# Kernel optimization log

Hardware: AMD Instinct MI355X
Metric: run time of the kernel (lower is better)

The kernel has to match this reference:

```python
import jax, jax.numpy as jnp
import numpy as np


def setup_inputs() -> dict:
    key = jax.random.key(0)
    x = jax.random.uniform(key, (16, 3, 224, 224), dtype=jnp.float32)
    return {"x": x, "timesteps": 32, "burst_length": 3, "interburst_interval": 5}


def reference(x, timesteps, burst_length, interburst_interval):
    period = burst_length + interburst_interval  # 8
    max_bursts = timesteps // period             # 4
    x_norm = jnp.clip(x, 0.0, 1.0)
    # floor(x * max_bursts) == torch .long() cast for non-negative values
    n_bursts = jnp.floor(x_norm * max_bursts)    # [B, *input_shape], float

    t = jnp.arange(timesteps)                    # [T]
    burst_idx = (t // period).astype(x.dtype)    # which burst each timestep belongs to
    within_burst = (t % period) < burst_length   # [T] bool

    # reshape time axis to broadcast at position 1: [1, T, 1, ..., 1]
    tshape = (1, timesteps) + (1,) * (x.ndim - 1)
    burst_idx = burst_idx.reshape(tshape)
    within_burst = within_burst.reshape(tshape)

    nb = jnp.expand_dims(n_bursts, 1)            # [B, 1, *input_shape]
    spikes = (within_burst & (burst_idx < nb)).astype(jnp.float32)
    return spikes  # [B, T, *input_shape]
```

## Files before the change

kernel.cpp:

```cpp
#include <hip/hip_runtime.h>


__global__ __launch_bounds__(256) void burst_coding_kernel(
    const float* __restrict__ x, float* __restrict__ out,
    const int* __restrict__ p_bl, const int* __restrict__ p_ibi,
    int T, int S4)
{
    const int bl     = *p_bl;
    const int period = bl + *p_ibi;
    const int maxb   = T / period;

    const int bt   = blockIdx.y;
    const int t    = bt % T;
    const int b    = bt / T;
    const int tm   = t % period;
    const int bidx = t / period;

    const int s4 = blockIdx.x * blockDim.x + threadIdx.x;
    if (s4 >= S4) return;

    float4* op = reinterpret_cast<float4*>(out) + (long)bt * S4 + s4;

    if (tm >= bl || bidx >= maxb) {
        *op = make_float4(0.f, 0.f, 0.f, 0.f);
        return;
    }

    const float mbf  = (float)maxb;
    const float bthr = (float)(bidx + 1);
    const float4 xv  = reinterpret_cast<const float4*>(x)[(long)b * S4 + s4];

    float4 v;
    v.x = (fminf(fmaxf(xv.x, 0.f), 1.f) * mbf >= bthr) ? 1.f : 0.f;
    v.y = (fminf(fmaxf(xv.y, 0.f), 1.f) * mbf >= bthr) ? 1.f : 0.f;
    v.z = (fminf(fmaxf(xv.z, 0.f), 1.f) * mbf >= bthr) ? 1.f : 0.f;
    v.w = (fminf(fmaxf(xv.w, 0.f), 1.f) * mbf >= bthr) ? 1.f : 0.f;
    *op = v;
}

extern "C" void kernel_launch(void* const* d_in, const int* in_sizes, int n_in,
                              void* d_out, int out_size, void* d_ws, size_t ws_size,
                              hipStream_t stream) {
    const float* x   = (const float*)d_in[0];
    const int* p_bl  = (const int*)d_in[2];
    const int* p_ibi = (const int*)d_in[3];
    float* out = (float*)d_out;

    const long N  = (long)in_sizes[0];
    const int  T  = (int)((long)out_size / N);
    const int  S  = 3 * 224 * 224;
    const int  S4 = S / 4;
    const int  B  = (int)(N / S);

    const int threads = 256;
    dim3 grid((S4 + threads - 1) / threads,
              (unsigned)(B * T));

    burst_coding_kernel<<<grid, dim3(threads), 0, stream>>>(
        x, out, p_bl, p_ibi, T, S4);
}
```

Before: 53.83 us.

## Split burst coding into a zero-fill kernel and a per-pixel active-burst kernel

Replaces the single kernel, which launched one grid row per (batch, timestep) and re-read x for every active timestep, with two kernels. One writes zeros to the inactive timesteps, two float4 per thread, and its blocks for active timesteps return at once. The other reads each x element once and writes all active timestep slices in a loop. This cuts repeated input reads and per-thread index math. It adds a second launch and loops with many strided writes in the active kernel.

New measurement: 60.12 us. 1.12x slower.

```diff
diff --git a/kernel.cpp b/kernel.cpp
--- a/kernel.cpp
+++ b/kernel.cpp
@@ -1,8 +1,10 @@
 #include <hip/hip_runtime.h>
 
 
-__global__ __launch_bounds__(256) void burst_coding_kernel(
-    const float* __restrict__ x, float* __restrict__ out,
+typedef float f32x4 __attribute__((ext_vector_type(4)));
+
+__global__ __launch_bounds__(256) void burst_zero_kernel(
+    float* __restrict__ out,
     const int* __restrict__ p_bl, const int* __restrict__ p_ibi,
     int T, int S4)
 {
@@ -12,30 +14,52 @@
 
     const int bt   = blockIdx.y;
     const int t    = bt % T;
-    const int b    = bt / T;
     const int tm   = t % period;
     const int bidx = t / period;
+    if (tm < bl && bidx < maxb) return;
 
+    const int s4a = blockIdx.x * (blockDim.x * 2) + threadIdx.x;
+    const int s4b = s4a + blockDim.x;
+
+    f32x4* op = reinterpret_cast<f32x4*>(out) + (long)bt * S4;
+    const f32x4 z = {0.f, 0.f, 0.f, 0.f};
+    if (s4a < S4) op[s4a] = z;
+    if (s4b < S4) op[s4b] = z;
+}
+
+__global__ __launch_bounds__(256) void burst_active_kernel(
+    const float* __restrict__ x, float* __restrict__ out,
+    const int* __restrict__ p_bl, const int* __restrict__ p_ibi,
+    int T, int S4)
+{
+    const int bl     = *p_bl;
+    const int period = bl + *p_ibi;
+    const int maxb   = T / period;
+    const float mbf  = (float)maxb;
+
+    const int b  = blockIdx.y;
     const int s4 = blockIdx.x * blockDim.x + threadIdx.x;
     if (s4 >= S4) return;
 
-    float4* op = reinterpret_cast<float4*>(out) + (long)bt * S4 + s4;
+    const f32x4 xv = reinterpret_cast<const f32x4*>(x)[(long)b * S4 + s4];
+    const float n0 = fminf(fmaxf(xv.x, 0.f), 1.f) * mbf;
+    const float n1 = fminf(fmaxf(xv.y, 0.f), 1.f) * mbf;
+    const float n2 = fminf(fmaxf(xv.z, 0.f), 1.f) * mbf;
+    const float n3 = fminf(fmaxf(xv.w, 0.f), 1.f) * mbf;
 
-    if (tm >= bl || bidx >= maxb) {
-        *op = make_float4(0.f, 0.f, 0.f, 0.f);
-        return;
+    f32x4* outp = reinterpret_cast<f32x4*>(out) + (long)b * T * S4 + s4;
+
+    for (int k = 0; k < maxb; ++k) {
+        const float thr = (float)(k + 1);
+        f32x4 v;
+        v.x = (n0 >= thr) ? 1.f : 0.f;
+        v.y = (n1 >= thr) ? 1.f : 0.f;
+        v.z = (n2 >= thr) ? 1.f : 0.f;
+        v.w = (n3 >= thr) ? 1.f : 0.f;
+        const long base = (long)(k * period) * S4;
+        for (int j = 0; j < bl; ++j)
+            outp[base + (long)j * S4] = v;
     }
-
-    const float mbf  = (float)maxb;
-    const float bthr = (float)(bidx + 1);
-    const float4 xv  = reinterpret_cast<const float4*>(x)[(long)b * S4 + s4];
-
-    float4 v;
-    v.x = (fminf(fmaxf(xv.x, 0.f), 1.f) * mbf >= bthr) ? 1.f : 0.f;
-    v.y = (fminf(fmaxf(xv.y, 0.f), 1.f) * mbf >= bthr) ? 1.f : 0.f;
-    v.z = (fminf(fmaxf(xv.z, 0.f), 1.f) * mbf >= bthr) ? 1.f : 0.f;
-    v.w = (fminf(fmaxf(xv.w, 0.f), 1.f) * mbf >= bthr) ? 1.f : 0.f;
-    *op = v;
 }
 
 extern "C" void kernel_launch(void* const* d_in, const int* in_sizes, int n_in,
@@ -53,9 +77,12 @@
     const int  B  = (int)(N / S);
 
     const int threads = 256;
-    dim3 grid((S4 + threads - 1) / threads,
-              (unsigned)(B * T));
 
-    burst_coding_kernel<<<grid, dim3(threads), 0, stream>>>(
-        x, out, p_bl, p_ibi, T, S4);
+    dim3 gz((S4 + threads * 2 - 1) / (threads * 2),
+            (unsigned)(B * T));
+    burst_zero_kernel<<<gz, dim3(threads), 0, stream>>>(out, p_bl, p_ibi, T, S4);
+
+    dim3 ga((S4 + threads - 1) / threads,
+            (unsigned)B);
+    burst_active_kernel<<<ga, dim3(threads), 0, stream>>>(x, out, p_bl, p_ibi, T, S4);
 }
```
